# Performance work log

Hardware: AMD Instinct MI355X
Metric: run time of the kernel (lower is better)

Reference implementation:

```python
import jax, jax.numpy as jnp
import numpy as np

K_SIZE = 5
PAD = 2  # (dilation*(k-1)+1-stride+1)//2 with dilation=stride=1
DEPTH_MAX = 10.0
SAMPLE_NUM = 40
AREA_TYPE = 1
AREA_THRED = 0.0  # k_size**2 * 0.5 * 0.0


def _select_index(k_size=K_SIZE, sample_num=SAMPLE_NUM, area_thred=AREA_THRED,
                  area_type=AREA_TYPE, seed=0):
    """Faithful port of AdaptiveDepth2normal.select_index (host-side, deterministic seed)."""
    rng = np.random.RandomState(seed)
    num = k_size ** 2
    p1 = rng.choice(num, sample_num, replace=True); rng.shuffle(p1)
    p2 = rng.choice(num, sample_num, replace=True); rng.shuffle(p2)
    p3 = rng.choice(num, sample_num, replace=True); rng.shuffle(p3)
    index_list = np.stack([p1, p2, p3], axis=1)
    valid_list, seen, areas = [], set(), []
    for row in index_list:
        a, b, c = np.sort(row)
        if (a, b, c) in seen:
            continue
        ax, ay = a % k_size, a // k_size
        bx, by = b % k_size, b // k_size
        cx, cy = c % k_size, c // k_size
        # NOTE: /2 applies only to second term, exactly as in the original code
        area = (bx - ax) * (cy - ay) - (by - ay) * (cx - ax) / 2
        if area > area_thred:
            valid_list.append([a, b, c]); seen.add((a, b, c)); areas.append(area)
        elif area < -area_thred:
            valid_list.append([a, c, b]); seen.add((a, c, b)); areas.append(-area)
    tri = np.asarray(valid_list, dtype=np.int32)              # [nn, 3]
    w = np.asarray(areas, dtype=np.float64) ** area_type
    return tri, (w / w.sum()).astype(np.float32)


def _unfold(x, k=K_SIZE, pad=PAD):
    """torch.nn.Unfold(k, padding=pad, stride=1): x [B,C,H,W] -> [B,C,k*k,H,W], kh-major order."""
    B, C, H, W = x.shape
    xp = jnp.pad(x, ((0, 0), (0, 0), (pad, pad), (pad, pad)))
    return jnp.stack([xp[:, :, dy:dy + H, dx:dx + W]
                      for dy in range(k) for dx in range(k)], axis=2)


def setup_inputs() -> dict:
    key = jax.random.key(0)
    k1, k2 = jax.random.split(key)
    B, H, W = 2, 384, 512
    depth = jax.random.uniform(k1, (B, 1, H, W), dtype=jnp.float32) * 8.0 + 0.5  # in (0, depth_max)
    Kmat = jnp.array([[500.0, 0.0, W / 2.0],
                      [0.0, 500.0, H / 2.0],
                      [0.0, 0.0, 1.0]], dtype=jnp.float32)
    intrinsic = jnp.tile(Kmat[None], (B, 1, 1))
    guide_weight = jax.random.uniform(k2, (B, H, W, K_SIZE * K_SIZE), dtype=jnp.float32)
    tri, aw = _select_index()
    return {"depth": depth, "intrinsic": intrinsic, "guide_weight": guide_weight,
            "triangle_index": jnp.asarray(tri), "triangle_area_weights": jnp.asarray(aw)}


def reference(depth, intrinsic, guide_weight, triangle_index, triangle_area_weights):
    d = depth[:, 0]                                  # [B,H,W]
    B, H, W = d.shape
    Kinv = jnp.linalg.inv(intrinsic)                 # [B,3,3]
    jj = jnp.arange(W, dtype=d.dtype)
    ii = jnp.arange(H, dtype=d.dtype)
    coords = jnp.stack([jnp.broadcast_to(jj[None, :], (H, W)),
                        jnp.broadcast_to(ii[:, None], (H, W)),
                        jnp.ones((H, W), d.dtype)], axis=0)  # [3,H,W] (u,v,1)
    points = jnp.einsum('bij,jhw->bihw', Kinv, coords) * d[:, None]  # [B,3,H,W]

    pp = _unfold(points).transpose(0, 3, 4, 2, 1)    # [B,H,W,25,3]
    p1 = jnp.take(pp, triangle_index[:, 0], axis=3)  # [B,H,W,nn,3]
    p2 = jnp.take(pp, triangle_index[:, 1], axis=3)
    p3 = jnp.take(pp, triangle_index[:, 2], axis=3)
    n = jnp.cross(p2 - p1, p3 - p1)                  # [B,H,W,nn,3]
    n = n / (jnp.linalg.norm(n, axis=-1, keepdims=True) + 1e-5)

    valid = ((d > 0) & (d < DEPTH_MAX)).astype(d.dtype)          # [B,H,W]
    vp = _unfold(valid[:, None])[:, 0].transpose(0, 2, 3, 1)     # [B,H,W,25]
    v_tri = (jnp.take(vp, triangle_index[:, 0], axis=3)
             * jnp.take(vp, triangle_index[:, 1], axis=3)
             * jnp.take(vp, triangle_index[:, 2], axis=3))       # [B,H,W,nn]
    g_tri = (jnp.take(guide_weight, triangle_index[:, 0], axis=3)
             * jnp.take(guide_weight, triangle_index[:, 1], axis=3)
             * jnp.take(guide_weight, triangle_index[:, 2], axis=3))
    fw = v_tri * triangle_area_weights[None, None, None, :] * g_tri  # if_area=True, if_pa=True
    fw = jax.nn.softmax(fw, axis=-1)
    nw = jnp.sum(n * fw[..., None], axis=3)                      # [B,H,W,3]
    nw = nw / (jnp.linalg.norm(nw, axis=-1, keepdims=True) + 1e-5)
    out = jnp.where(valid[..., None] > 0, nw, jnp.zeros((), d.dtype))
    return out.transpose(0, 3, 1, 2), points
```

## Files before the change

### kernel.cpp

```cpp
#include <hip/hip_runtime.h>
#include <math.h>

#define KSZ 5
#define PADR 2
#define TILE_W 32
#define TILE_H 8
#define HALO_W (TILE_W + 2*PADR)
#define HALO_H (TILE_H + 2*PADR)
#define HALO_N (HALO_H * HALO_W)
#define MAX_TRI 128
#define NTHREADS 256

__device__ __forceinline__ float eigen_pexp(float x) {
    float m = floorf(__fmaf_rn(x, 1.44269504088896341f, 0.5f));
    float r = __fmaf_rn(-m, 0.693359375f, x);
    r = __fmaf_rn(-m, -2.12194440e-4f, r);
    float r2 = __fmul_rn(r, r);
    float p = 1.9875691500E-4f;
    p = __fmaf_rn(p, r, 1.3981999507E-3f);
    p = __fmaf_rn(p, r, 8.3334519073E-3f);
    p = __fmaf_rn(p, r, 4.1665795894E-2f);
    p = __fmaf_rn(p, r, 1.6666665459E-1f);
    p = __fmaf_rn(p, r, 5.0000001201E-1f);
    p = __fmaf_rn(p, r2, r);
    p = __fadd_rn(p, 1.0f);
    return ldexpf(p, (int)m);
}

__global__ __launch_bounds__(NTHREADS)
void pts_kernel(const float* __restrict__ depth,
                const float* __restrict__ intrinsic,
                float4* __restrict__ pts,
                float* __restrict__ out_p,
                int B, int H, int W)
{
    const int HP = H + 2*PADR, WP = W + 2*PADR;
    const int total = B * HP * WP;
    int idx = blockIdx.x * NTHREADS + threadIdx.x;
    if (idx >= total) return;
    int b   = idx / (HP * WP);
    int rem = idx - b * (HP * WP);
    int pr  = rem / WP;
    int pc  = rem - pr * WP;
    int hh  = pr - PADR;
    int ww  = pc - PADR;

    const float* Km = intrinsic + b * 9;
    const double a00=Km[0], a01=Km[1], a02=Km[2];
    const double a10=Km[3], a11=Km[4], a12=Km[5];
    const double a20=Km[6], a21=Km[7], a22=Km[8];
    const double det = a00*(a11*a22-a12*a21) - a01*(a10*a22-a12*a20) + a02*(a10*a21-a11*a20);
    const double id  = 1.0 / det;
    const float i00 = (float)((a11*a22-a12*a21)*id), i01 = (float)((a02*a21-a01*a22)*id), i02 = (float)((a01*a12-a02*a11)*id);
    const float i10 = (float)((a12*a20-a10*a22)*id), i11 = (float)((a00*a22-a02*a20)*id), i12 = (float)((a02*a10-a00*a12)*id);
    const float i20 = (float)((a10*a21-a11*a20)*id), i21 = (float)((a01*a20-a00*a21)*id), i22 = (float)((a00*a11-a01*a10)*id);

    float4 v = make_float4(0.f, 0.f, 0.f, 0.f);
    if (hh >= 0 && hh < H && ww >= 0 && ww < W) {
        float d  = depth[(size_t)(b * H + hh) * W + ww];
        float fj = (float)ww, fi = (float)hh;
        float sx = __fadd_rn(__fadd_rn(__fmul_rn(i00, fj), __fmul_rn(i01, fi)), i02);
        float sy = __fadd_rn(__fadd_rn(__fmul_rn(i10, fj), __fmul_rn(i11, fi)), i12);
        float sz = __fadd_rn(__fadd_rn(__fmul_rn(i20, fj), __fmul_rn(i21, fi)), i22);
        v.x = __fmul_rn(sx, d);
        v.y = __fmul_rn(sy, d);
        v.z = __fmul_rn(sz, d);
        v.w = (d > 0.f && d < 10.f) ? 1.f : 0.f;
        const size_t hw = (size_t)H * W;
        const size_t p0 = (size_t)b * 3 * hw + (size_t)hh * W + ww;
        out_p[p0]        = v.x;
        out_p[p0 + hw]   = v.y;
        out_p[p0 + 2*hw] = v.z;
    }
    pts[idx] = v;
}

__global__ __launch_bounds__(NTHREADS)
void d2n_main(const float4* __restrict__ pts,
              const float* __restrict__ guide,
              const int* __restrict__ tri,
              const float* __restrict__ aw,
              float* __restrict__ out_n,
              int B, int H, int W, int T)
{
    __shared__ float s_gw[TILE_H * TILE_W * (KSZ*KSZ)];

    const int HP = H + 2*PADR, WP = W + 2*PADR;
    const int tid = threadIdx.x;
    const int tx  = tid & (TILE_W - 1);
    const int ty  = tid >> 5;
    const int b   = blockIdx.z;
    const int w0  = blockIdx.x * TILE_W;
    const int h0  = blockIdx.y * TILE_H;

    const int GW_TOT = TILE_H * TILE_W * (KSZ*KSZ);
    for (int i = tid; i < GW_TOT; i += NTHREADS) {
        int r   = i / (TILE_W * KSZ*KSZ);
        int rem = i - r * (TILE_W * KSZ*KSZ);
        int hh  = h0 + r;
        float val = 0.f;
        if (hh < H)
            val = guide[((size_t)(b * H + hh) * W + w0) * (KSZ*KSZ) + rem];
        s_gw[i] = val;
    }
    __syncthreads();

    const float* gw_pix = &s_gw[(ty * TILE_W + tx) * (KSZ*KSZ)];
    const int pbase = (b * HP + h0 + ty) * WP + (w0 + tx);

    const int Tl = T < MAX_TRI ? T : MAX_TRI;

    float r0=0.f, r1=0.f, r2=0.f, r3=0.f, r4=0.f, r5=0.f, r6=0.f, r7=0.f;
    float axv = 0.f, ayv = 0.f, azv = 0.f;

    auto body = [&](int t, float& racc) {
        int j1 = tri[3*t], j2 = tri[3*t+1], j3 = tri[3*t+2];
        float awt = aw[t];
        int o1 = (j1 / KSZ) * WP + (j1 - (j1 / KSZ) * KSZ);
        int o2 = (j2 / KSZ) * WP + (j2 - (j2 / KSZ) * KSZ);
        int o3 = (j3 / KSZ) * WP + (j3 - (j3 / KSZ) * KSZ);
        float4 p1 = pts[pbase + o1];
        float4 p2 = pts[pbase + o2];
        float4 p3 = pts[pbase + o3];
        float vv = __fmul_rn(__fmul_rn(p1.w, p2.w), p3.w);
        float g  = __fmul_rn(__fmul_rn(gw_pix[j1], gw_pix[j2]), gw_pix[j3]);
        float f  = __fmul_rn(__fmul_rn(vv, awt), g);
        float e  = eigen_pexp(f);
        racc = __fadd_rn(racc, e);
        float e1x = __fsub_rn(p2.x, p1.x), e1y = __fsub_rn(p2.y, p1.y), e1z = __fsub_rn(p2.z, p1.z);
        float e2x = __fsub_rn(p3.x, p1.x), e2y = __fsub_rn(p3.y, p1.y), e2z = __fsub_rn(p3.z, p1.z);
        float t1 = __fmul_rn(e1z, e2y);
        float nx = __fmaf_rn(e1y, e2z, -t1);
        float t2 = __fmul_rn(e1x, e2z);
        float ny = __fmaf_rn(e1z, e2x, -t2);
        float t3 = __fmul_rn(e1y, e2x);
        float nz = __fmaf_rn(e1x, e2y, -t3);
        float q   = __fmaf_rn(nx, nx, __fmaf_rn(ny, ny, __fmul_rn(nz, nz)));
        float den = __fadd_rn(__builtin_amdgcn_sqrtf(q), 1e-5f);
        float inv = __builtin_amdgcn_rcpf(den);
        float ew  = __fmul_rn(e, inv);
        axv = __fmaf_rn(nx, ew, axv);
        ayv = __fmaf_rn(ny, ew, ayv);
        azv = __fmaf_rn(nz, ew, azv);
    };

    const int nmain = (Tl >= 8) ? (Tl & ~7) : 0;
    for (int tb = 0; tb < nmain; tb += 8) {
        body(tb+0, r0); body(tb+1, r1); body(tb+2, r2); body(tb+3, r3);
        body(tb+4, r4); body(tb+5, r5); body(tb+6, r6); body(tb+7, r7);
    }
    float s = 0.f;
    if (Tl >= 8)
        s = __fadd_rn(__fadd_rn(__fadd_rn(r0, r1), __fadd_rn(r2, r3)),
                      __fadd_rn(__fadd_rn(r4, r5), __fadd_rn(r6, r7)));
    for (int t = nmain; t < Tl; ++t) body(t, s);

    const float4 pc = pts[pbase + PADR * WP + PADR];
    float nwx = __fdiv_rn(axv, s);
    float nwy = __fdiv_rn(ayv, s);
    float nwz = __fdiv_rn(azv, s);
    float q2   = __fmaf_rn(nwx, nwx, __fmaf_rn(nwy, nwy, __fmul_rn(nwz, nwz)));
    float den2 = __fadd_rn(__fsqrt_rn(q2), 1e-5f);
    float ox = __fdiv_rn(nwx, den2);
    float oy = __fdiv_rn(nwy, den2);
    float oz = __fdiv_rn(nwz, den2);
    if (pc.w <= 0.f) { ox = 0.f; oy = 0.f; oz = 0.f; }

    const int hh = h0 + ty, ww = w0 + tx;
    if (hh < H && ww < W) {
        const size_t hw = (size_t)H * W;
        const size_t p0 = (size_t)b * 3 * hw + (size_t)hh * W + ww;
        out_n[p0]        = ox;
        out_n[p0 + hw]   = oy;
        out_n[p0 + 2*hw] = oz;
    }
}

__global__ __launch_bounds__(NTHREADS)
void d2n_fallback(const float* __restrict__ depth,
                  const float* __restrict__ intrinsic,
                  const float* __restrict__ guide,
                  const int* __restrict__ tri,
                  const float* __restrict__ aw,
                  float* __restrict__ out_n,
                  float* __restrict__ out_p,
                  int B, int H, int W, int T)
{
    __shared__ float4 s_pts[HALO_N];
    __shared__ float  s_gw[TILE_H * TILE_W * (KSZ*KSZ)];

    const int tid = threadIdx.x;
    const int tx  = tid & (TILE_W - 1);
    const int ty  = tid >> 5;
    const int b   = blockIdx.z;
    const int w0  = blockIdx.x * TILE_W;
    const int h0  = blockIdx.y * TILE_H;

    const float* Km = intrinsic + b * 9;
    const double a00=Km[0], a01=Km[1], a02=Km[2];
    const double a10=Km[3], a11=Km[4], a12=Km[5];
    const double a20=Km[6], a21=Km[7], a22=Km[8];
    const double det = a00*(a11*a22-a12*a21) - a01*(a10*a22-a12*a20) + a02*(a10*a21-a11*a20);
    const double id  = 1.0 / det;
    const float i00 = (float)((a11*a22-a12*a21)*id), i01 = (float)((a02*a21-a01*a22)*id), i02 = (float)((a01*a12-a02*a11)*id);
    const float i10 = (float)((a12*a20-a10*a22)*id), i11 = (float)((a00*a22-a02*a20)*id), i12 = (float)((a02*a10-a00*a12)*id);
    const float i20 = (float)((a10*a21-a11*a20)*id), i21 = (float)((a01*a20-a00*a21)*id), i22 = (float)((a00*a11-a01*a10)*id);

    for (int i = tid; i < HALO_N; i += NTHREADS) {
        int r  = i / HALO_W;
        int c  = i - r * HALO_W;
        int hh = h0 + r - PADR;
        int ww = w0 + c - PADR;
        float4 v = make_float4(0.f, 0.f, 0.f, 0.f);
        if (hh >= 0 && hh < H && ww >= 0 && ww < W) {
            float d  = depth[(size_t)(b * H + hh) * W + ww];
            float fj = (float)ww, fi = (float)hh;
            float sx = __fadd_rn(__fadd_rn(__fmul_rn(i00, fj), __fmul_rn(i01, fi)), i02);
            float sy = __fadd_rn(__fadd_rn(__fmul_rn(i10, fj), __fmul_rn(i11, fi)), i12);
            float sz = __fadd_rn(__fadd_rn(__fmul_rn(i20, fj), __fmul_rn(i21, fi)), i22);
            v.x = __fmul_rn(sx, d);
            v.y = __fmul_rn(sy, d);
            v.z = __fmul_rn(sz, d);
            v.w = (d > 0.f && d < 10.f) ? 1.f : 0.f;
        }
        s_pts[i] = v;
    }
    const int GW_TOT = TILE_H * TILE_W * (KSZ*KSZ);
    for (int i = tid; i < GW_TOT; i += NTHREADS) {
        int r   = i / (TILE_W * KSZ*KSZ);
        int rem = i - r * (TILE_W * KSZ*KSZ);
        int hh  = h0 + r;
        float val = 0.f;
        if (hh < H)
            val = guide[((size_t)(b * H + hh) * W + w0) * (KSZ*KSZ) + rem];
        s_gw[i] = val;
    }
    __syncthreads();

    const int base = ty * HALO_W + tx;
    const int ctr  = base + PADR * HALO_W + PADR;
    const float* gw_pix = &s_gw[(ty * TILE_W + tx) * (KSZ*KSZ)];
    const float4 pcv = s_pts[ctr];
    const int Tl = T < MAX_TRI ? T : MAX_TRI;

    float r0=0.f, r1=0.f, r2=0.f, r3=0.f, r4=0.f, r5=0.f, r6=0.f, r7=0.f;
    float axv = 0.f, ayv = 0.f, azv = 0.f;
    auto body = [&](int t, float& racc) {
        int j1 = tri[3*t], j2 = tri[3*t+1], j3 = tri[3*t+2];
        float awt = aw[t];
        int o1 = base + (j1 / KSZ) * HALO_W + (j1 - (j1 / KSZ) * KSZ);
        int o2 = base + (j2 / KSZ) * HALO_W + (j2 - (j2 / KSZ) * KSZ);
        int o3 = base + (j3 / KSZ) * HALO_W + (j3 - (j3 / KSZ) * KSZ);
        float4 p1 = s_pts[o1], p2 = s_pts[o2], p3 = s_pts[o3];
        float vv = __fmul_rn(__fmul_rn(p1.w, p2.w), p3.w);
        float g  = __fmul_rn(__fmul_rn(gw_pix[j1], gw_pix[j2]), gw_pix[j3]);
        float f  = __fmul_rn(__fmul_rn(vv, awt), g);
        float e  = eigen_pexp(f);
        racc = __fadd_rn(racc, e);
        float e1x = __fsub_rn(p2.x, p1.x), e1y = __fsub_rn(p2.y, p1.y), e1z = __fsub_rn(p2.z, p1.z);
        float e2x = __fsub_rn(p3.x, p1.x), e2y = __fsub_rn(p3.y, p1.y), e2z = __fsub_rn(p3.z, p1.z);
        float t1 = __fmul_rn(e1z, e2y);
        float nx = __fmaf_rn(e1y, e2z, -t1);
        float t2 = __fmul_rn(e1x, e2z);
        float ny = __fmaf_rn(e1z, e2x, -t2);
        float t3 = __fmul_rn(e1y, e2x);
        float nz = __fmaf_rn(e1x, e2y, -t3);
        float q   = __fmaf_rn(nx, nx, __fmaf_rn(ny, ny, __fmul_rn(nz, nz)));
        float den = __fadd_rn(__builtin_amdgcn_sqrtf(q), 1e-5f);
        float inv = __builtin_amdgcn_rcpf(den);
        float ew  = __fmul_rn(e, inv);
        axv = __fmaf_rn(nx, ew, axv);
        ayv = __fmaf_rn(ny, ew, ayv);
        azv = __fmaf_rn(nz, ew, azv);
    };
    const int nmain = (Tl >= 8) ? (Tl & ~7) : 0;
    for (int tb = 0; tb < nmain; tb += 8) {
        body(tb+0, r0); body(tb+1, r1); body(tb+2, r2); body(tb+3, r3);
        body(tb+4, r4); body(tb+5, r5); body(tb+6, r6); body(tb+7, r7);
    }
    float s = 0.f;
    if (Tl >= 8)
        s = __fadd_rn(__fadd_rn(__fadd_rn(r0, r1), __fadd_rn(r2, r3)),
                      __fadd_rn(__fadd_rn(r4, r5), __fadd_rn(r6, r7)));
    for (int t = nmain; t < Tl; ++t) body(t, s);

    float nwx = __fdiv_rn(axv, s);
    float nwy = __fdiv_rn(ayv, s);
    float nwz = __fdiv_rn(azv, s);
    float q2   = __fmaf_rn(nwx, nwx, __fmaf_rn(nwy, nwy, __fmul_rn(nwz, nwz)));
    float den2 = __fadd_rn(__fsqrt_rn(q2), 1e-5f);
    float ox = __fdiv_rn(nwx, den2);
    float oy = __fdiv_rn(nwy, den2);
    float oz = __fdiv_rn(nwz, den2);
    if (pcv.w <= 0.f) { ox = 0.f; oy = 0.f; oz = 0.f; }

    const int hh = h0 + ty, ww = w0 + tx;
    if (hh < H && ww < W) {
        const size_t hw = (size_t)H * W;
        const size_t p0 = (size_t)b * 3 * hw + (size_t)hh * W + ww;
        out_n[p0]        = ox;
        out_n[p0 + hw]   = oy;
        out_n[p0 + 2*hw] = oz;
        out_p[p0]        = pcv.x;
        out_p[p0 + hw]   = pcv.y;
        out_p[p0 + 2*hw] = pcv.z;
    }
}

extern "C" void kernel_launch(void* const* d_in, const int* in_sizes, int n_in,
                              void* d_out, int out_size, void* d_ws, size_t ws_size,
                              hipStream_t stream) {
    const float* depth = (const float*)d_in[0];
    const float* intr  = (const float*)d_in[1];
    const float* guide = (const float*)d_in[2];
    const int*   tri   = (const int*)d_in[3];
    const float* aw    = (const float*)d_in[4];

    const int B = in_sizes[1] / 9;
    const int T = in_sizes[4];
    const int H = 384, W = 512;
    const int HP = H + 2*PADR, WP = W + 2*PADR;

    float* out_n = (float*)d_out;
    float* out_p = out_n + (size_t)B * 3 * H * W;

    const size_t need = (size_t)B * HP * WP * sizeof(float4);
    dim3 grid((W + TILE_W - 1) / TILE_W, (H + TILE_H - 1) / TILE_H, B);

    if (ws_size >= need) {
        float4* pts = (float4*)d_ws;
        int total = B * HP * WP;
        pts_kernel<<<(total + NTHREADS - 1) / NTHREADS, NTHREADS, 0, stream>>>(
            depth, intr, pts, out_p, B, H, W);
        d2n_main<<<grid, NTHREADS, 0, stream>>>(
            pts, guide, tri, aw, out_n, B, H, W, T);
    } else {
        d2n_fallback<<<grid, NTHREADS, 0, stream>>>(
            depth, intr, guide, tri, aw, out_n, out_p, B, H, W, T);
    }
}
```

Before: 47.29 us.

## Premultiply validity into shared guide weights and software-pipeline triangle loads

pts_kernel now also writes a separate per-pixel validity buffer. d2n_main folds that validity into the shared-memory guide weights, so each triangle no longer multiplies three validity values. The triangle loop is restructured into a two-stage software pipeline that loads the next triangle's indices, points and weights while computing the current one. This aims to hide global load latency and drop some multiplies, at the cost of an extra buffer write and read and higher register pressure. The rounding order changes slightly, since validity is multiplied into g before the area weight.

```diff
diff --git a/kernel.cpp b/kernel.cpp
--- a/kernel.cpp
+++ b/kernel.cpp
@@ -31,6 +31,7 @@
 void pts_kernel(const float* __restrict__ depth,
                 const float* __restrict__ intrinsic,
                 float4* __restrict__ pts,
+                float* __restrict__ vbuf,
                 float* __restrict__ out_p,
                 int B, int H, int W)
 {
@@ -72,11 +73,13 @@
         out_p[p0 + hw]   = v.y;
         out_p[p0 + 2*hw] = v.z;
     }
-    pts[idx] = v;
+    pts[idx]  = v;
+    vbuf[idx] = v.w;
 }
 
 __global__ __launch_bounds__(NTHREADS)
 void d2n_main(const float4* __restrict__ pts,
+              const float* __restrict__ vbuf,
               const float* __restrict__ guide,
               const int* __restrict__ tri,
               const float* __restrict__ aw,
@@ -95,65 +98,86 @@
 
     const int GW_TOT = TILE_H * TILE_W * (KSZ*KSZ);
     for (int i = tid; i < GW_TOT; i += NTHREADS) {
-        int r   = i / (TILE_W * KSZ*KSZ);
-        int rem = i - r * (TILE_W * KSZ*KSZ);
-        int hh  = h0 + r;
+        int row = i / (TILE_W * 25);
+        int rem = i - row * (TILE_W * 25);
+        int col = rem / 25;
+        int k   = rem - col * 25;
+        int hh  = h0 + row;
         float val = 0.f;
         if (hh < H)
-            val = guide[((size_t)(b * H + hh) * W + w0) * (KSZ*KSZ) + rem];
-        s_gw[i] = val;
+            val = guide[((size_t)(b * H + hh) * W + w0) * 25 + rem];
+        int kd = k / 5, km = k - 5 * kd;
+        float pv = vbuf[(size_t)(b * HP + h0 + row + kd) * WP + (w0 + col + km)];
+        s_gw[i] = __fmul_rn(val, pv);
     }
     __syncthreads();
 
     const float* gw_pix = &s_gw[(ty * TILE_W + tx) * (KSZ*KSZ)];
     const int pbase = (b * HP + h0 + ty) * WP + (w0 + tx);
-
     const int Tl = T < MAX_TRI ? T : MAX_TRI;
+    const int tlast = Tl - 1;
 
     float r0=0.f, r1=0.f, r2=0.f, r3=0.f, r4=0.f, r5=0.f, r6=0.f, r7=0.f;
     float axv = 0.f, ayv = 0.f, azv = 0.f;
 
-    auto body = [&](int t, float& racc) {
-        int j1 = tri[3*t], j2 = tri[3*t+1], j3 = tri[3*t+2];
-        float awt = aw[t];
-        int o1 = (j1 / KSZ) * WP + (j1 - (j1 / KSZ) * KSZ);
-        int o2 = (j2 / KSZ) * WP + (j2 - (j2 / KSZ) * KSZ);
-        int o3 = (j3 / KSZ) * WP + (j3 - (j3 / KSZ) * KSZ);
-        float4 p1 = pts[pbase + o1];
-        float4 p2 = pts[pbase + o2];
-        float4 p3 = pts[pbase + o3];
-        float vv = __fmul_rn(__fmul_rn(p1.w, p2.w), p3.w);
-        float g  = __fmul_rn(__fmul_rn(gw_pix[j1], gw_pix[j2]), gw_pix[j3]);
-        float f  = __fmul_rn(__fmul_rn(vv, awt), g);
-        float e  = eigen_pexp(f);
-        racc = __fadd_rn(racc, e);
-        float e1x = __fsub_rn(p2.x, p1.x), e1y = __fsub_rn(p2.y, p1.y), e1z = __fsub_rn(p2.z, p1.z);
-        float e2x = __fsub_rn(p3.x, p1.x), e2y = __fsub_rn(p3.y, p1.y), e2z = __fsub_rn(p3.z, p1.z);
-        float t1 = __fmul_rn(e1z, e2y);
-        float nx = __fmaf_rn(e1y, e2z, -t1);
-        float t2 = __fmul_rn(e1x, e2z);
-        float ny = __fmaf_rn(e1z, e2x, -t2);
-        float t3 = __fmul_rn(e1y, e2x);
-        float nz = __fmaf_rn(e1x, e2y, -t3);
-        float q   = __fmaf_rn(nx, nx, __fmaf_rn(ny, ny, __fmul_rn(nz, nz)));
-        float den = __fadd_rn(__builtin_amdgcn_sqrtf(q), 1e-5f);
-        float inv = __builtin_amdgcn_rcpf(den);
-        float ew  = __fmul_rn(e, inv);
-        axv = __fmaf_rn(nx, ew, axv);
-        ayv = __fmaf_rn(ny, ew, ayv);
-        azv = __fmaf_rn(nz, ew, azv);
-    };
-
+    float4 Ap1, Ap2, Ap3; float Ag1, Ag2, Ag3, Aaw;
+    float4 Bp1, Bp2, Bp3; float Bg1, Bg2, Bg3, Baw;
+
+#define LOADT(tt, P1, P2, P3, G1, G2, G3, AWT) {                       \
+    int j1_ = tri[3*(tt)], j2_ = tri[3*(tt)+1], j3_ = tri[3*(tt)+2];   \
+    AWT = aw[tt];                                                      \
+    G1 = gw_pix[j1_]; G2 = gw_pix[j2_]; G3 = gw_pix[j3_];              \
+    P1 = pts[pbase + (j1_ / KSZ) * WP + (j1_ - (j1_ / KSZ) * KSZ)];    \
+    P2 = pts[pbase + (j2_ / KSZ) * WP + (j2_ - (j2_ / KSZ) * KSZ)];    \
+    P3 = pts[pbase + (j3_ / KSZ) * WP + (j3_ - (j3_ / KSZ) * KSZ)];    \
+}
+
+#define COMPUTE(RACC, P1, P2, P3, G1, G2, G3, AWT) {                   \
+    float g = __fmul_rn(__fmul_rn(G1, G2), G3);                        \
+    float f = __fmul_rn(g, AWT);                                       \
+    float e = eigen_pexp(f);                                           \
+    RACC = __fadd_rn(RACC, e);                                         \
+    float e1x = __fsub_rn(P2.x, P1.x), e1y = __fsub_rn(P2.y, P1.y), e1z = __fsub_rn(P2.z, P1.z); \
+    float e2x = __fsub_rn(P3.x, P1.x), e2y = __fsub_rn(P3.y, P1.y), e2z = __fsub_rn(P3.z, P1.z); \
+    float t1 = __fmul_rn(e1z, e2y);                                    \
+    float nx = __fmaf_rn(e1y, e2z, -t1);                               \
+    float t2 = __fmul_rn(e1x, e2z);                                    \
+    float ny = __fmaf_rn(e1z, e2x, -t2);                               \
+    float t3 = __fmul_rn(e1y, e2x);                                    \
+    float nz = __fmaf_rn(e1x, e2y, -t3);                               \
+    float q   = __fmaf_rn(nx, nx, __fmaf_rn(ny, ny, __fmul_rn(nz, nz))); \
+    float den = __fadd_rn(__builtin_amdgcn_sqrtf(q), 1e-5f);           \
+    float inv = __builtin_amdgcn_rcpf(den);                            \
+    float ew  = __fmul_rn(e, inv);                                     \
+    axv = __fmaf_rn(nx, ew, axv);                                      \
+    ayv = __fmaf_rn(ny, ew, ayv);                                      \
+    azv = __fmaf_rn(nz, ew, azv);                                      \
+}
+
+#define BODY_A(tn, RACC) { LOADT(tn, Bp1,Bp2,Bp3,Bg1,Bg2,Bg3,Baw); COMPUTE(RACC, Ap1,Ap2,Ap3,Ag1,Ag2,Ag3,Aaw); }
+#define BODY_B(tn, RACC) { LOADT(tn, Ap1,Ap2,Ap3,Ag1,Ag2,Ag3,Aaw); COMPUTE(RACC, Bp1,Bp2,Bp3,Bg1,Bg2,Bg3,Baw); }
+
+    LOADT(0, Ap1,Ap2,Ap3,Ag1,Ag2,Ag3,Aaw);
     const int nmain = (Tl >= 8) ? (Tl & ~7) : 0;
     for (int tb = 0; tb < nmain; tb += 8) {
-        body(tb+0, r0); body(tb+1, r1); body(tb+2, r2); body(tb+3, r3);
-        body(tb+4, r4); body(tb+5, r5); body(tb+6, r6); body(tb+7, r7);
+        int t1c = tb+1 < Tl ? tb+1 : tlast;  int t2c = tb+2 < Tl ? tb+2 : tlast;
+        int t3c = tb+3 < Tl ? tb+3 : tlast;  int t4c = tb+4 < Tl ? tb+4 : tlast;
+        int t5c = tb+5 < Tl ? tb+5 : tlast;  int t6c = tb+6 < Tl ? tb+6 : tlast;
+        int t7c = tb+7 < Tl ? tb+7 : tlast;  int t8c = tb+8 < Tl ? tb+8 : tlast;
+        BODY_A(t1c, r0); BODY_B(t2c, r1);
+        BODY_A(t3c, r2); BODY_B(t4c, r3);
+        BODY_A(t5c, r4); BODY_B(t6c, r5);
+        BODY_A(t7c, r6); BODY_B(t8c, r7);
     }
     float s = 0.f;
     if (Tl >= 8)
         s = __fadd_rn(__fadd_rn(__fadd_rn(r0, r1), __fadd_rn(r2, r3)),
                       __fadd_rn(__fadd_rn(r4, r5), __fadd_rn(r6, r7)));
-    for (int t = nmain; t < Tl; ++t) body(t, s);
+    for (int t = nmain; t < Tl; ++t) {
+        int tn = t+1 < Tl ? t+1 : tlast;
+        if ((t - nmain) & 1) { BODY_B(tn, s); }
+        else                 { BODY_A(tn, s); }
+    }
 
     const float4 pc = pts[pbase + PADR * WP + PADR];
     float nwx = __fdiv_rn(axv, s);
@@ -174,6 +198,10 @@
         out_n[p0 + hw]   = oy;
         out_n[p0 + 2*hw] = oz;
     }
+#undef BODY_A
+#undef BODY_B
+#undef LOADT
+#undef COMPUTE
 }
 
 __global__ __launch_bounds__(NTHREADS)
@@ -324,16 +352,18 @@
     float* out_n = (float*)d_out;
     float* out_p = out_n + (size_t)B * 3 * H * W;
 
-    const size_t need = (size_t)B * HP * WP * sizeof(float4);
+    const size_t n_pad  = (size_t)B * HP * WP;
+    const size_t need   = n_pad * (sizeof(float4) + sizeof(float));
     dim3 grid((W + TILE_W - 1) / TILE_W, (H + TILE_H - 1) / TILE_H, B);
 
     if (ws_size >= need) {
-        float4* pts = (float4*)d_ws;
-        int total = B * HP * WP;
+        float4* pts  = (float4*)d_ws;
+        float*  vbuf = (float*)(pts + n_pad);
+        int total = (int)n_pad;
         pts_kernel<<<(total + NTHREADS - 1) / NTHREADS, NTHREADS, 0, stream>>>(
-            depth, intr, pts, out_p, B, H, W);
+            depth, intr, pts, vbuf, out_p, B, H, W);
         d2n_main<<<grid, NTHREADS, 0, stream>>>(
-            pts, guide, tri, aw, out_n, B, H, W, T);
+            pts, vbuf, guide, tri, aw, out_n, B, H, W, T);
     } else {
         d2n_fallback<<<grid, NTHREADS, 0, stream>>>(
             depth, intr, guide, tri, aw, out_n, out_p, B, H, W, T);
```

After: 59.43 us. +25.7%, slower.

## Split points into SoA planes, fold validity into guide weights, use fast exp

Applied to the files above, without the earlier changes.

The padded point buffer changes from float4 AoS to three separate X/Y/Z float planes. The validity mask is no longer stored per point; it is recomputed from depth during the shared-memory guide load and multiplied into the cached guide weights, so the per-triangle validity product disappears. The polynomial exp is replaced with the hardware __expf intrinsic, which may change rounding slightly relative to the reference. Each triangle now issues nine scalar loads instead of three vector loads, in exchange for a smaller workspace.

```diff
diff --git a/kernel.cpp b/kernel.cpp
--- a/kernel.cpp
+++ b/kernel.cpp
@@ -11,26 +11,12 @@
 #define MAX_TRI 128
 #define NTHREADS 256
 
-__device__ __forceinline__ float eigen_pexp(float x) {
-    float m = floorf(__fmaf_rn(x, 1.44269504088896341f, 0.5f));
-    float r = __fmaf_rn(-m, 0.693359375f, x);
-    r = __fmaf_rn(-m, -2.12194440e-4f, r);
-    float r2 = __fmul_rn(r, r);
-    float p = 1.9875691500E-4f;
-    p = __fmaf_rn(p, r, 1.3981999507E-3f);
-    p = __fmaf_rn(p, r, 8.3334519073E-3f);
-    p = __fmaf_rn(p, r, 4.1665795894E-2f);
-    p = __fmaf_rn(p, r, 1.6666665459E-1f);
-    p = __fmaf_rn(p, r, 5.0000001201E-1f);
-    p = __fmaf_rn(p, r2, r);
-    p = __fadd_rn(p, 1.0f);
-    return ldexpf(p, (int)m);
-}
 
 __global__ __launch_bounds__(NTHREADS)
 void pts_kernel(const float* __restrict__ depth,
                 const float* __restrict__ intrinsic,
-                float4* __restrict__ pts,
+                float* __restrict__ Xp, float* __restrict__ Yp,
+                float* __restrict__ Zp,
                 float* __restrict__ out_p,
                 int B, int H, int W)
 {
@@ -55,28 +41,29 @@
     const float i10 = (float)((a12*a20-a10*a22)*id), i11 = (float)((a00*a22-a02*a20)*id), i12 = (float)((a02*a10-a00*a12)*id);
     const float i20 = (float)((a10*a21-a11*a20)*id), i21 = (float)((a01*a20-a00*a21)*id), i22 = (float)((a00*a11-a01*a10)*id);
 
-    float4 v = make_float4(0.f, 0.f, 0.f, 0.f);
+    float x = 0.f, y = 0.f, z = 0.f;
     if (hh >= 0 && hh < H && ww >= 0 && ww < W) {
         float d  = depth[(size_t)(b * H + hh) * W + ww];
         float fj = (float)ww, fi = (float)hh;
         float sx = __fadd_rn(__fadd_rn(__fmul_rn(i00, fj), __fmul_rn(i01, fi)), i02);
         float sy = __fadd_rn(__fadd_rn(__fmul_rn(i10, fj), __fmul_rn(i11, fi)), i12);
         float sz = __fadd_rn(__fadd_rn(__fmul_rn(i20, fj), __fmul_rn(i21, fi)), i22);
-        v.x = __fmul_rn(sx, d);
-        v.y = __fmul_rn(sy, d);
-        v.z = __fmul_rn(sz, d);
-        v.w = (d > 0.f && d < 10.f) ? 1.f : 0.f;
+        x = __fmul_rn(sx, d);
+        y = __fmul_rn(sy, d);
+        z = __fmul_rn(sz, d);
         const size_t hw = (size_t)H * W;
         const size_t p0 = (size_t)b * 3 * hw + (size_t)hh * W + ww;
-        out_p[p0]        = v.x;
-        out_p[p0 + hw]   = v.y;
-        out_p[p0 + 2*hw] = v.z;
-    }
-    pts[idx] = v;
+        out_p[p0]        = x;
+        out_p[p0 + hw]   = y;
+        out_p[p0 + 2*hw] = z;
+    }
+    Xp[idx] = x; Yp[idx] = y; Zp[idx] = z;
 }
 
 __global__ __launch_bounds__(NTHREADS)
-void d2n_main(const float4* __restrict__ pts,
+void d2n_main(const float* __restrict__ Xp, const float* __restrict__ Yp,
+              const float* __restrict__ Zp,
+              const float* __restrict__ depth,
               const float* __restrict__ guide,
               const int* __restrict__ tri,
               const float* __restrict__ aw,
@@ -95,19 +82,28 @@
 
     const int GW_TOT = TILE_H * TILE_W * (KSZ*KSZ);
     for (int i = tid; i < GW_TOT; i += NTHREADS) {
-        int r   = i / (TILE_W * KSZ*KSZ);
-        int rem = i - r * (TILE_W * KSZ*KSZ);
-        int hh  = h0 + r;
+        int row = i / (TILE_W * 25);
+        int rem = i - row * (TILE_W * 25);
+        int col = rem / 25;
+        int k   = rem - col * 25;
+        int hh  = h0 + row;
         float val = 0.f;
         if (hh < H)
-            val = guide[((size_t)(b * H + hh) * W + w0) * (KSZ*KSZ) + rem];
-        s_gw[i] = val;
+            val = guide[((size_t)(b * H + hh) * W + w0) * 25 + rem];
+        int kd = k / 5, km = k - 5 * kd;
+        int hh2 = hh + kd - PADR;
+        int ww2 = w0 + col + km - PADR;
+        float pv = 0.f;
+        if (hh2 >= 0 && hh2 < H && ww2 >= 0 && ww2 < W) {
+            float d = depth[(size_t)(b * H + hh2) * W + ww2];
+            pv = (d > 0.f && d < 10.f) ? 1.f : 0.f;
+        }
+        s_gw[i] = __fmul_rn(val, pv);
     }
     __syncthreads();
 
     const float* gw_pix = &s_gw[(ty * TILE_W + tx) * (KSZ*KSZ)];
     const int pbase = (b * HP + h0 + ty) * WP + (w0 + tx);
-
     const int Tl = T < MAX_TRI ? T : MAX_TRI;
 
     float r0=0.f, r1=0.f, r2=0.f, r3=0.f, r4=0.f, r5=0.f, r6=0.f, r7=0.f;
@@ -119,16 +115,15 @@
         int o1 = (j1 / KSZ) * WP + (j1 - (j1 / KSZ) * KSZ);
         int o2 = (j2 / KSZ) * WP + (j2 - (j2 / KSZ) * KSZ);
         int o3 = (j3 / KSZ) * WP + (j3 - (j3 / KSZ) * KSZ);
-        float4 p1 = pts[pbase + o1];
-        float4 p2 = pts[pbase + o2];
-        float4 p3 = pts[pbase + o3];
-        float vv = __fmul_rn(__fmul_rn(p1.w, p2.w), p3.w);
-        float g  = __fmul_rn(__fmul_rn(gw_pix[j1], gw_pix[j2]), gw_pix[j3]);
-        float f  = __fmul_rn(__fmul_rn(vv, awt), g);
-        float e  = eigen_pexp(f);
+        float p1x = Xp[pbase + o1], p1y = Yp[pbase + o1], p1z = Zp[pbase + o1];
+        float p2x = Xp[pbase + o2], p2y = Yp[pbase + o2], p2z = Zp[pbase + o2];
+        float p3x = Xp[pbase + o3], p3y = Yp[pbase + o3], p3z = Zp[pbase + o3];
+        float g = __fmul_rn(__fmul_rn(gw_pix[j1], gw_pix[j2]), gw_pix[j3]);
+        float f = __fmul_rn(g, awt);
+        float e = __expf(f);
         racc = __fadd_rn(racc, e);
-        float e1x = __fsub_rn(p2.x, p1.x), e1y = __fsub_rn(p2.y, p1.y), e1z = __fsub_rn(p2.z, p1.z);
-        float e2x = __fsub_rn(p3.x, p1.x), e2y = __fsub_rn(p3.y, p1.y), e2z = __fsub_rn(p3.z, p1.z);
+        float e1x = __fsub_rn(p2x, p1x), e1y = __fsub_rn(p2y, p1y), e1z = __fsub_rn(p2z, p1z);
+        float e2x = __fsub_rn(p3x, p1x), e2y = __fsub_rn(p3y, p1y), e2z = __fsub_rn(p3z, p1z);
         float t1 = __fmul_rn(e1z, e2y);
         float nx = __fmaf_rn(e1y, e2z, -t1);
         float t2 = __fmul_rn(e1x, e2z);
@@ -155,7 +150,12 @@
                       __fadd_rn(__fadd_rn(r4, r5), __fadd_rn(r6, r7)));
     for (int t = nmain; t < Tl; ++t) body(t, s);
 
-    const float4 pc = pts[pbase + PADR * WP + PADR];
+    const int hh = h0 + ty, ww = w0 + tx;
+    float cd = 0.f;
+    if (hh < H && ww < W)
+        cd = depth[(size_t)(b * H + hh) * W + ww];
+    const bool cvalid = (cd > 0.f && cd < 10.f);
+
     float nwx = __fdiv_rn(axv, s);
     float nwy = __fdiv_rn(ayv, s);
     float nwz = __fdiv_rn(azv, s);
@@ -164,9 +164,8 @@
     float ox = __fdiv_rn(nwx, den2);
     float oy = __fdiv_rn(nwy, den2);
     float oz = __fdiv_rn(nwz, den2);
-    if (pc.w <= 0.f) { ox = 0.f; oy = 0.f; oz = 0.f; }
-
-    const int hh = h0 + ty, ww = w0 + tx;
+    if (!cvalid) { ox = 0.f; oy = 0.f; oz = 0.f; }
+
     if (hh < H && ww < W) {
         const size_t hw = (size_t)H * W;
         const size_t p0 = (size_t)b * 3 * hw + (size_t)hh * W + ww;
@@ -255,7 +254,7 @@
         float vv = __fmul_rn(__fmul_rn(p1.w, p2.w), p3.w);
         float g  = __fmul_rn(__fmul_rn(gw_pix[j1], gw_pix[j2]), gw_pix[j3]);
         float f  = __fmul_rn(__fmul_rn(vv, awt), g);
-        float e  = eigen_pexp(f);
+        float e  = __expf(f);
         racc = __fadd_rn(racc, e);
         float e1x = __fsub_rn(p2.x, p1.x), e1y = __fsub_rn(p2.y, p1.y), e1z = __fsub_rn(p2.z, p1.z);
         float e2x = __fsub_rn(p3.x, p1.x), e2y = __fsub_rn(p3.y, p1.y), e2z = __fsub_rn(p3.z, p1.z);
@@ -324,16 +323,19 @@
     float* out_n = (float*)d_out;
     float* out_p = out_n + (size_t)B * 3 * H * W;
 
-    const size_t need = (size_t)B * HP * WP * sizeof(float4);
+    const size_t n_pad = (size_t)B * HP * WP;
+    const size_t need  = 3 * n_pad * sizeof(float);
     dim3 grid((W + TILE_W - 1) / TILE_W, (H + TILE_H - 1) / TILE_H, B);
 
     if (ws_size >= need) {
-        float4* pts = (float4*)d_ws;
-        int total = B * HP * WP;
+        float* Xp = (float*)d_ws;
+        float* Yp = Xp + n_pad;
+        float* Zp = Yp + n_pad;
+        int total = (int)n_pad;
         pts_kernel<<<(total + NTHREADS - 1) / NTHREADS, NTHREADS, 0, stream>>>(
-            depth, intr, pts, out_p, B, H, W);
+            depth, intr, Xp, Yp, Zp, out_p, B, H, W);
         d2n_main<<<grid, NTHREADS, 0, stream>>>(
-            pts, guide, tri, aw, out_n, B, H, W, T);
+            Xp, Yp, Zp, depth, guide, tri, aw, out_n, B, H, W, T);
     } else {
         d2n_fallback<<<grid, NTHREADS, 0, stream>>>(
             depth, intr, guide, tri, aw, out_n, out_p, B, H, W, T);
```

After: 63.07 us. 33.4% more time.
